# Kernel tuning notes

Hardware: AMD Instinct MI355X
Metric: run time of the kernel (lower is better)

## Reference

```python
import jax, jax.numpy as jnp
import numpy as np

IOU_TH = 0.5      # iou_threshold
SCORE_TH = 0.5    # confidence_threshold (passed as score_threshold to tf NMS)
MAX_DET = 512     # max_detections


def setup_inputs() -> dict:
    key = jax.random.key(0)
    k1, k2, k3 = jax.random.split(key, 3)
    B, N, C = 8, 2048, 80
    # tf.image.non_max_suppression interprets box columns as corners
    # (y1, x1, y2, x2); generate valid corner boxes in [0, 1].
    mins = jax.random.uniform(k1, (B, N, 2), dtype=jnp.float32)
    sizes = jax.random.uniform(k2, (B, N, 2), dtype=jnp.float32) * 0.2 + 0.01
    box_prediction = jnp.concatenate([mins, mins + sizes], axis=-1)  # [B,N,4]
    class_prediction = jax.random.normal(k3, (B, N, C), dtype=jnp.float32) * 2.0
    return {"box_prediction": box_prediction, "class_prediction": class_prediction}


def _nms_single(boxes, cls_pred, conf):
    """Greedy NMS for one image. boxes [N,4], cls_pred [N,C], conf [N].
    Matches tf.image.non_max_suppression semantics (corner-coordinate IoU,
    score threshold, greedy suppression in descending score order),
    then gathers boxes/cls/conf at the kept indices, padded to MAX_DET."""
    N = boxes.shape[0]
    order = jnp.argsort(-conf)                 # descending scores
    b = boxes[order]                            # [N,4]
    c = cls_pred[order]                         # [N,C]
    s = conf[order]                             # [N]

    bb = jax.lax.stop_gradient(b)               # IoU/indices are non-diff
    y1, x1, y2, x2 = bb[:, 0], bb[:, 1], bb[:, 2], bb[:, 3]
    area = (y2 - y1) * (x2 - x1)                # [N]
    ih = jnp.clip(jnp.minimum(y2[:, None], y2[None, :]) -
                  jnp.maximum(y1[:, None], y1[None, :]), 0.0)
    iw = jnp.clip(jnp.minimum(x2[:, None], x2[None, :]) -
                  jnp.maximum(x1[:, None], x1[None, :]), 0.0)
    inter = ih * iw                             # [N,N]
    union = area[:, None] + area[None, :] - inter
    iou = inter / jnp.maximum(union, 1e-9)      # [N,N]

    valid = s > SCORE_TH                        # score_threshold filter
    idxs = jnp.arange(N)

    def step(keep, xs):
        row, i = xs
        # if box i survives, suppress all later boxes overlapping > IOU_TH
        sup = (row > IOU_TH) & (idxs > i) & keep[i]
        return keep & ~sup, None

    keep, _ = jax.lax.scan(step, valid, (iou, idxs))

    # select kept boxes (already sorted by score) padded to MAX_DET
    masked = jnp.where(keep, s, -1.0)
    top_s, top_idx = jax.lax.top_k(jax.lax.stop_gradient(masked), MAX_DET)
    vm = top_s > SCORE_TH                       # validity of each output slot
    out_box = b[top_idx] * vm[:, None].astype(b.dtype)
    out_cls = c[top_idx] * vm[:, None].astype(c.dtype)
    out_conf = jnp.where(vm, s[top_idx], 0.0)
    return out_box, out_cls, out_conf


def reference(box_prediction, class_prediction):
    # from_logits=True branch of the layer
    class_confidence = jnp.max(jax.nn.sigmoid(class_prediction), axis=-1)  # [B,N]
    cls_prob = jax.nn.softmax(class_prediction, axis=-1)                   # [B,N,C]
    nms_box, nms_cls, nms_conf = jax.vmap(_nms_single)(
        box_prediction, cls_prob, class_confidence)
    return nms_box, nms_cls, nms_conf
```

## Files before the change

kernel.cpp:

```cpp
#include <hip/hip_runtime.h>
#include <stdint.h>

#define BB 8
#define NN 2048
#define NC 80
#define MAXDET 512
#define WPR 32


#define ORD_HALF 0xBF000000u

__global__ __launch_bounds__(64) void k_conf(const float* __restrict__ cls,
                                             uint64_t* __restrict__ keys) {
    int gid = blockIdx.x * 64 + threadIdx.x;
    const float4* p = (const float4*)(cls + (size_t)gid * NC);
    float m = -3.0e38f;
#pragma unroll
    for (int i = 0; i < NC / 4; ++i) {
        float4 v = p[i];
        m = fmaxf(m, fmaxf(fmaxf(v.x, v.y), fmaxf(v.z, v.w)));
    }
    float e  = expf(-m);
    float cf = 1.0f / (1.0f + e);
    uint32_t u = __float_as_uint(cf);
    u = (u & 0x80000000u) ? ~u : (u | 0x80000000u);
    int n = gid & (NN - 1);
    keys[gid] = ((uint64_t)u << 32) | (uint32_t)(NN - 1 - n);
}

#define RCHUNK 128
__global__ __launch_bounds__(512) void k_rank(const uint64_t* __restrict__ keys_in,
                                              uint64_t* __restrict__ keys_out,
                                              const float* __restrict__ boxes,
                                              float* __restrict__ sboxes) {
    __shared__ uint64_t sk[NN];
    __shared__ uint16_t part[4][RCHUNK];
    int b = blockIdx.y, t = threadIdx.x;
    const uint64_t* kin = keys_in + (size_t)b * NN;
#pragma unroll
    for (int j = 0; j < NN / 512; ++j)
        sk[t + j * 512] = kin[t + j * 512];
    __syncthreads();
    int sub = t >> 7;
    int el  = t & (RCHUNK - 1);
    int e   = blockIdx.x * RCHUNK + el;
    uint64_t mykey = sk[e];
    int base = sub * (NN / 4);
    int r = 0;
    for (int mm = 0; mm < NN / 4; ++mm)
        r += (sk[base + mm] > mykey) ? 1 : 0;
    part[sub][el] = (uint16_t)r;
    __syncthreads();
    if (t < RCHUNK) {
        int rank = part[0][t] + part[1][t] + part[2][t] + part[3][t];
        keys_out[(size_t)b * NN + rank] = mykey;
        int orig = (NN - 1) - (int)(mykey & 0xFFFFFFFFull);
        ((float4*)sboxes)[(size_t)b * NN + rank] =
            ((const float4*)boxes)[(size_t)b * NN + orig];
    }
}

__global__ void k_sup(const float* __restrict__ sboxes, uint64_t* __restrict__ sup,
                      uint64_t* __restrict__ diagw) {
#pragma clang fp contract(off)
    __shared__ float cy1[256], cx1[256], cy2[256], cx2[256], car[256];
    __shared__ float ry1[64], rx1[64], ry2[64], rx2[64], rar[64];
    int rt = blockIdx.x, ct = blockIdx.y, b = blockIdx.z;
    int t = threadIdx.x;
    int col0 = ct << 8, row0 = rt << 6;
    {
        float4 bx = ((const float4*)sboxes)[(size_t)b * NN + col0 + t];
        cy1[t] = bx.x; cx1[t] = bx.y; cy2[t] = bx.z; cx2[t] = bx.w;
        car[t] = (bx.z - bx.x) * (bx.w - bx.y);
        if (t < 64) {
            float4 rb = ((const float4*)sboxes)[(size_t)b * NN + row0 + t];
            ry1[t] = rb.x; rx1[t] = rb.y; ry2[t] = rb.z; rx2[t] = rb.w;
            rar[t] = (rb.z - rb.x) * (rb.w - rb.y);
        }
    }
    __syncthreads();
    int lr = t & 63, lg = t >> 6;
    int r = row0 + lr;
    int gw = (ct << 2) + lg;
    int cbase = gw << 6;
    uint64_t w = 0;
    if (cbase + 63 > r) {
        float y1 = ry1[lr], x1 = rx1[lr], y2 = ry2[lr], x2 = rx2[lr], ar = rar[lr];
        int lcb = lg << 6;
        for (int c = 0; c < 64; ++c) {
            int lc = lcb + c;
            float ih = fmaxf(fminf(y2, cy2[lc]) - fmaxf(y1, cy1[lc]), 0.0f);
            float iw = fmaxf(fminf(x2, cx2[lc]) - fmaxf(x1, cx1[lc]), 0.0f);
            float inter = ih * iw;
            float uni = (ar + car[lc]) - inter;
            float iou = inter / fmaxf(uni, 1e-9f);
            if ((iou > 0.5f) & ((cbase + c) > r)) w |= (1ull << c);
        }
    }
    sup[((size_t)b * NN + r) * WPR + gw] = w;
    if (gw == (r >> 6)) diagw[(size_t)b * NN + r] = w;
}

__global__ __launch_bounds__(64) void k_nms(const uint64_t* __restrict__ keys,
                                            const float* __restrict__ sboxes,
                                            const uint64_t* __restrict__ sup,
                                            const uint64_t* __restrict__ diagw,
                                            int* __restrict__ kidx,
                                            int* __restrict__ kcount,
                                            float* __restrict__ out_box,
                                            float* __restrict__ out_conf) {
    __shared__ uint64_t dg[NN];
    __shared__ uint64_t kmaskS[WPR];
    __shared__ int pfx[WPR];
    __shared__ int s_kc;
    int b = blockIdx.x, t = threadIdx.x;
    const uint64_t* supb = sup + (size_t)b * NN * WPR;
    const uint64_t* keyb = keys + (size_t)b * NN;
    const uint64_t* dgb  = diagw + (size_t)b * NN;

    for (int i = t; i < NN; i += 64) dg[i] = dgb[i];
    if (t < WPR) kmaskS[t] = 0;

    uint64_t kb = 0;
    for (int i = 0; i < WPR; ++i) {
        uint32_t hi = (uint32_t)(keyb[(i << 6) + t] >> 32);
        uint64_t bal = __ballot(hi > ORD_HALF);
        if (t == i) kb = ~bal;
    }
    __syncthreads();

    int l2 = t & 31, half = t >> 5;
    int cnt = 0;
    for (int g = 0; g < WPR; ++g) {
        uint64_t diag = dg[(g << 6) + t];
        uint32_t dlo = (uint32_t)diag, dhi = (uint32_t)(diag >> 32);
        const uint64_t* rowp = supb + ((size_t)((g << 6) + (half << 5)) * WPR) + l2;
        uint64_t rows[32];
#pragma unroll
        for (int j = 0; j < 32; ++j) rows[j] = rowp[(size_t)j * WPR];
        uint64_t rwv = __shfl(kb, g);
        uint32_t rw_lo = __builtin_amdgcn_readfirstlane((uint32_t)rwv);
        uint32_t rw_hi = __builtin_amdgcn_readfirstlane((uint32_t)(rwv >> 32));
        uint32_t gm_lo = 0, gm_hi = 0;
#pragma unroll
        for (int c = 0; c < 32; ++c) {
            uint32_t rlo = __builtin_amdgcn_readlane(dlo, c);
            uint32_t rhi = __builtin_amdgcn_readlane(dhi, c);
            if (((rw_lo >> c) & 1u) == 0u) {
                rw_lo |= rlo; rw_hi |= rhi; gm_lo |= (1u << c);
            }
        }
#pragma unroll
        for (int c = 0; c < 32; ++c) {
            uint32_t rlo = __builtin_amdgcn_readlane(dlo, c + 32);
            uint32_t rhi = __builtin_amdgcn_readlane(dhi, c + 32);
            if (((rw_hi >> c) & 1u) == 0u) {
                rw_lo |= rlo; rw_hi |= rhi; gm_hi |= (1u << c);
            }
        }
        uint64_t gm = ((uint64_t)gm_hi << 32) | gm_lo;
        uint32_t gmh = half ? gm_hi : gm_lo;
        uint64_t acc = 0;
#pragma unroll
        for (int j = 0; j < 32; ++j)
            acc |= (((gmh >> j) & 1u) ? rows[j] : 0ull);
        acc |= __shfl(acc, t ^ 32);
        if (t < 32) kb |= acc;
        if (t == 0) kmaskS[g] = gm;
        cnt += __popcll(gm);
        if (cnt >= MAXDET) break;
    }
    __syncthreads();

    if (t == 0) {
        int s = 0;
        for (int w2 = 0; w2 < WPR; ++w2) { pfx[w2] = s; s += __popcll(kmaskS[w2]); }
        s_kc = (s < MAXDET) ? s : MAXDET;
        kcount[b] = s_kc;
    }
    __syncthreads();
    for (int i = t; i < NN; i += 64) {
        uint64_t m = kmaskS[i >> 6];
        if ((m >> (i & 63)) & 1ull) {
            int rank = pfx[i >> 6] + __popcll(m & ((1ull << (i & 63)) - 1ull));
            if (rank < MAXDET) {
                ((float4*)out_box)[(size_t)b * MAXDET + rank] =
                    ((const float4*)sboxes)[(size_t)b * NN + i];
                uint64_t kk = keyb[i];
                uint32_t u = (uint32_t)(kk >> 32);
                float cf = (u & 0x80000000u) ? __uint_as_float(u ^ 0x80000000u)
                                             : __uint_as_float(~u);
                out_conf[(size_t)b * MAXDET + rank] = cf;
                kidx[b * MAXDET + rank] = (NN - 1) - (int)(kk & 0xFFFFFFFFull);
            }
        }
    }
    for (int k = s_kc + t; k < MAXDET; k += 64) {
        ((float4*)out_box)[(size_t)b * MAXDET + k] = make_float4(0.f, 0.f, 0.f, 0.f);
        out_conf[(size_t)b * MAXDET + k] = 0.0f;
    }
}

__global__ void k_softmax(const float* __restrict__ cls, const int* __restrict__ kidx,
                          const int* __restrict__ kcount, float* __restrict__ out_cls) {
    int k = blockIdx.x, b = blockIdx.y, lane = threadIdx.x;
    float* dst = out_cls + ((size_t)b * MAXDET + k) * NC;
    if (k >= kcount[b]) {
        dst[lane] = 0.0f;
        if (lane < NC - 64) dst[64 + lane] = 0.0f;
        return;
    }
    int n = kidx[b * MAXDET + k];
    const float* src = cls + ((size_t)b * NN + n) * NC;
    float x0 = src[lane];
    float x1 = (lane < NC - 64) ? src[64 + lane] : -3.0e38f;
    float m = fmaxf(x0, x1);
    for (int o = 32; o > 0; o >>= 1) m = fmaxf(m, __shfl_xor(m, o));
    float e0 = expf(x0 - m);
    float e1 = (lane < NC - 64) ? expf(x1 - m) : 0.0f;
    float s = e0 + e1;
    for (int o = 32; o > 0; o >>= 1) s += __shfl_xor(s, o);
    dst[lane] = e0 / s;
    if (lane < NC - 64) dst[64 + lane] = e1 / s;
}

extern "C" void kernel_launch(void* const* d_in, const int* in_sizes, int n_in,
                              void* d_out, int out_size, void* d_ws, size_t ws_size,
                              hipStream_t stream) {
    const float* boxes = (const float*)d_in[0];
    const float* cls   = (const float*)d_in[1];
    float* out      = (float*)d_out;
    float* out_box  = out;
    float* out_cls  = out + BB * MAXDET * 4;
    float* out_conf = out + BB * MAXDET * (4 + NC);

    char* ws = (char*)d_ws;
    uint64_t* keysA  = (uint64_t*)(ws + 0);
    uint64_t* keysB  = (uint64_t*)(ws + 131072);
    float*    sboxes = (float*)(ws + 262144);
    int*      kidx   = (int*)(ws + 524288);
    int*      kcount = (int*)(ws + 540672);
    uint64_t* diagw  = (uint64_t*)(ws + 540800);
    uint64_t* sup    = (uint64_t*)(ws + 671872);

    k_conf<<<(BB * NN) / 64, 64, 0, stream>>>(cls, keysA);
    k_rank<<<dim3(NN / RCHUNK, BB), 512, 0, stream>>>(keysA, keysB, boxes, sboxes);
    k_sup<<<dim3(NN / 64, NN / 256, BB), 256, 0, stream>>>(sboxes, sup, diagw);
    k_nms<<<BB, 64, 0, stream>>>(keysB, sboxes, sup, diagw, kidx, kcount, out_box, out_conf);
    k_softmax<<<dim3(MAXDET, BB), 64, 0, stream>>>(cls, kidx, kcount, out_cls);
}
```

Measured before the change: 86.29 us.

## Prefetch next NMS row block into registers and iterate only unsuppressed bits

The serial NMS block loop now double-buffers the 32 suppression-row words and the diagonal word for the next 64-box group in registers, so global loads overlap the current group's work. The diagonal is read straight from global memory, which removes the LDS staging array and its barrier. The fixed 64-step readlane scan is replaced by a ctz-driven loop that visits only surviving candidates. This costs more registers (64 extra uint64 values), which may lower occupancy or cause spills, and the new while loop has scalar, data-dependent control flow.

```diff
diff --git a/kernel.cpp b/kernel.cpp
--- a/kernel.cpp
+++ b/kernel.cpp
@@ -109,7 +109,6 @@
                                             int* __restrict__ kcount,
                                             float* __restrict__ out_box,
                                             float* __restrict__ out_conf) {
-    __shared__ uint64_t dg[NN];
     __shared__ uint64_t kmaskS[WPR];
     __shared__ int pfx[WPR];
     __shared__ int s_kc;
@@ -117,49 +116,48 @@
     const uint64_t* supb = sup + (size_t)b * NN * WPR;
     const uint64_t* keyb = keys + (size_t)b * NN;
     const uint64_t* dgb  = diagw + (size_t)b * NN;
-
-    for (int i = t; i < NN; i += 64) dg[i] = dgb[i];
     if (t < WPR) kmaskS[t] = 0;
 
     uint64_t kb = 0;
+#pragma unroll 8
     for (int i = 0; i < WPR; ++i) {
         uint32_t hi = (uint32_t)(keyb[(i << 6) + t] >> 32);
         uint64_t bal = __ballot(hi > ORD_HALF);
         if (t == i) kb = ~bal;
     }
-    __syncthreads();
 
     int l2 = t & 31, half = t >> 5;
+    uint64_t rows[32], rowsN[32];
+    uint64_t diag, diagN = 0;
+    {
+        const uint64_t* rowp = supb + (size_t)(half << 5) * WPR + l2;
+#pragma unroll
+        for (int j = 0; j < 32; ++j) rows[j] = rowp[(size_t)j * WPR];
+        diag = dgb[t];
+    }
+
     int cnt = 0;
     for (int g = 0; g < WPR; ++g) {
-        uint64_t diag = dg[(g << 6) + t];
+        if (g + 1 < WPR) {
+            const uint64_t* rowp = supb + (size_t)(((g + 1) << 6) + (half << 5)) * WPR + l2;
+#pragma unroll
+            for (int j = 0; j < 32; ++j) rowsN[j] = rowp[(size_t)j * WPR];
+            diagN = dgb[((g + 1) << 6) + t];
+        }
         uint32_t dlo = (uint32_t)diag, dhi = (uint32_t)(diag >> 32);
-        const uint64_t* rowp = supb + ((size_t)((g << 6) + (half << 5)) * WPR) + l2;
-        uint64_t rows[32];
-#pragma unroll
-        for (int j = 0; j < 32; ++j) rows[j] = rowp[(size_t)j * WPR];
         uint64_t rwv = __shfl(kb, g);
         uint32_t rw_lo = __builtin_amdgcn_readfirstlane((uint32_t)rwv);
         uint32_t rw_hi = __builtin_amdgcn_readfirstlane((uint32_t)(rwv >> 32));
-        uint32_t gm_lo = 0, gm_hi = 0;
-#pragma unroll
-        for (int c = 0; c < 32; ++c) {
+        uint64_t todo = ~(((uint64_t)rw_hi << 32) | rw_lo);
+        uint64_t gm = 0;
+        while (todo) {
+            int c = __builtin_ctzll(todo);
+            gm |= (1ull << c);
             uint32_t rlo = __builtin_amdgcn_readlane(dlo, c);
             uint32_t rhi = __builtin_amdgcn_readlane(dhi, c);
-            if (((rw_lo >> c) & 1u) == 0u) {
-                rw_lo |= rlo; rw_hi |= rhi; gm_lo |= (1u << c);
-            }
-        }
-#pragma unroll
-        for (int c = 0; c < 32; ++c) {
-            uint32_t rlo = __builtin_amdgcn_readlane(dlo, c + 32);
-            uint32_t rhi = __builtin_amdgcn_readlane(dhi, c + 32);
-            if (((rw_hi >> c) & 1u) == 0u) {
-                rw_lo |= rlo; rw_hi |= rhi; gm_hi |= (1u << c);
-            }
-        }
-        uint64_t gm = ((uint64_t)gm_hi << 32) | gm_lo;
-        uint32_t gmh = half ? gm_hi : gm_lo;
+            todo &= ~((((uint64_t)rhi << 32) | rlo) | (1ull << c));
+        }
+        uint32_t gmh = half ? (uint32_t)(gm >> 32) : (uint32_t)gm;
         uint64_t acc = 0;
 #pragma unroll
         for (int j = 0; j < 32; ++j)
@@ -168,6 +166,9 @@
         if (t < 32) kb |= acc;
         if (t == 0) kmaskS[g] = gm;
         cnt += __popcll(gm);
+#pragma unroll
+        for (int j = 0; j < 32; ++j) rows[j] = rowsN[j];
+        diag = diagN;
         if (cnt >= MAXDET) break;
     }
     __syncthreads();
```

New measurement: 86.94 us. Within noise of the previous version (+0.8%).
